# Kernel optimization log

Hardware: AMD Instinct MI355X
Metric: run time of the kernel (lower is better)

Reference implementation:

```python
import jax, jax.numpy as jnp
import numpy as np

K = 1000   # grid rows (detections from model 1, truncated to 1000)
N = 1000   # grid cols (detections from model 2)
M = 900000 # number of non-empty (overlapping) pairs
F = 7      # per-pair feature dim
SENTINEL = -9999.0


def setup_inputs() -> dict:
    key = jax.random.key(0)
    ks = jax.random.split(key, 12)
    def w(k, o, i):
        return jax.random.normal(k, (o, i), dtype=jnp.float32) * 0.05
    def b(k, o):
        return jax.random.normal(k, (o,), dtype=jnp.float32) * 0.05
    return {
        "input_1": jax.random.normal(ks[0], (1, F, 1, M), dtype=jnp.float32),
        "T_out": jnp.zeros((1, K, N), dtype=jnp.float32),
        "T_indices": jax.random.randint(ks[1], (2, M), 0, K),
        "w1": w(ks[2], 18, F),  "b1": b(ks[3], 18),
        "w2": w(ks[4], 36, 18), "b2": b(ks[5], 36),
        "w3": w(ks[6], 36, 36), "b3": b(ks[7], 36),
        "w4": w(ks[8], 1, 36),  "b4": b(ks[9], 1),
    }


def reference(input_1, T_out, T_indices, w1, b1, w2, b2, w3, b3, w4, b4):
    # 1x1 conv stack == channel matmuls on the flattened [F, M] features.
    x = input_1[0, :, 0, :]                       # [F, M]
    h = jax.nn.relu(w1 @ x + b1[:, None])         # [18, M]
    h = jax.nn.relu(w2 @ h + b2[:, None])         # [36, M]
    h = jax.nn.relu(w3 @ h + b3[:, None])         # [36, M]
    vals = (w4 @ h + b4[:, None])[0]              # [M]

    grid = jnp.full(T_out.shape, SENTINEL, dtype=T_out.dtype)  # [1, K, N]
    grid = grid.at[:, T_indices[0], T_indices[1]].set(vals[None, :])

    # MaxPool2d([1, N]) -> max over cols; MaxPool2d([K, 1]) -> max over rows.
    row_max = grid.max(axis=2).squeeze()          # [K]
    col_max = grid.max(axis=1).squeeze()          # [N]
    return (row_max, col_max)
```

## Files before the change

kernel.cpp:

```cpp
#include <hip/hip_runtime.h>
#include <stdint.h>

#define KK 1000
#define NN 1000
#define MM 900000
#define FF 7
#define SENTINEL -9999.0f

template <int N, typename F>
__device__ __forceinline__ void unroll_loop(F&& f) {
    if constexpr (N > 0) {
        unroll_loop<N - 1>(static_cast<F&&>(f));
        f(N - 1);
    }
}

__global__ __launch_bounds__(256) void init_grid(ulonglong2* __restrict__ g, int n2) {
    int i = blockIdx.x * 256 + threadIdx.x;
    if (i < n2) g[i] = make_ulonglong2(0ULL, 0ULL);
}

__global__ __launch_bounds__(256, 4) void mlp_scatter(
    const float* __restrict__ in,
    const int*   __restrict__ idx,
    const float* __restrict__ w1, const float* __restrict__ b1,
    const float* __restrict__ w2, const float* __restrict__ b2,
    const float* __restrict__ w3, const float* __restrict__ b3,
    const float* __restrict__ w4, const float* __restrict__ b4,
    unsigned long long* __restrict__ grid)
{
    int m = blockIdx.x * 256 + threadIdx.x;
    if (m >= MM) return;

    float x[FF];
    unroll_loop<FF>([&](int f) { x[f] = in[f * MM + m]; });

    float h1[18];
    unroll_loop<18>([&](int o) {
        float a = b1[o];
        unroll_loop<FF>([&](int i) { a = fmaf(w1[o * FF + i], x[i], a); });
        h1[o] = fmaxf(a, 0.0f);
    });

    float h2[36];
    unroll_loop<36>([&](int o) {
        float a = b2[o];
        unroll_loop<18>([&](int i) { a = fmaf(w2[o * 18 + i], h1[i], a); });
        h2[o] = fmaxf(a, 0.0f);
    });

    float v = b4[0];
    unroll_loop<36>([&](int o) {
        float a = b3[o];
        unroll_loop<36>([&](int i) { a = fmaf(w3[o * 36 + i], h2[i], a); });
        v = fmaf(w4[o], fmaxf(a, 0.0f), v);
    });

    int r = idx[m];
    int c = idx[MM + m];
    unsigned long long packed =
        ((unsigned long long)(unsigned)(m + 1) << 32) | (unsigned)__float_as_uint(v);
    atomicMax(&grid[r * NN + c], packed);
}

__global__ __launch_bounds__(256) void row_max_k(const unsigned long long* __restrict__ g,
                                                 float* __restrict__ out) {
    int r = blockIdx.x;
    float mx = SENTINEL;
    for (int c = threadIdx.x; c < NN; c += 256) {
        unsigned long long p = g[(size_t)r * NN + c];
        if (p) mx = fmaxf(mx, __uint_as_float((unsigned)p));
    }
    __shared__ float red[256];
    red[threadIdx.x] = mx;
    __syncthreads();
    for (int s = 128; s > 0; s >>= 1) {
        if (threadIdx.x < s) red[threadIdx.x] = fmaxf(red[threadIdx.x], red[threadIdx.x + s]);
        __syncthreads();
    }
    if (threadIdx.x == 0) out[r] = red[0];
}

#define CCHUNKS 25
#define CROWS   (KK / CCHUNKS)

__global__ __launch_bounds__(256) void col_partial(const unsigned long long* __restrict__ g,
                                                   float* __restrict__ part) {
    int n = blockIdx.x * 256 + threadIdx.x;
    if (n >= NN) return;
    int k0 = blockIdx.y * CROWS;
    float mx = SENTINEL;
    for (int k = k0; k < k0 + CROWS; ++k) {
        unsigned long long p = g[(size_t)k * NN + n];
        if (p) mx = fmaxf(mx, __uint_as_float((unsigned)p));
    }
    part[blockIdx.y * NN + n] = mx;
}

__global__ __launch_bounds__(256) void col_final(const float* __restrict__ part,
                                                 float* __restrict__ out) {
    int n = blockIdx.x * 256 + threadIdx.x;
    if (n >= NN) return;
    float mx = SENTINEL;
#pragma unroll
    for (int c = 0; c < CCHUNKS; ++c) mx = fmaxf(mx, part[c * NN + n]);
    out[KK + n] = mx;
}

extern "C" void kernel_launch(void* const* d_in, const int* in_sizes, int n_in,
                              void* d_out, int out_size, void* d_ws, size_t ws_size,
                              hipStream_t stream) {
    const float* in  = (const float*)d_in[0];
    const int*   idx = (const int*)d_in[2];
    const float* w1  = (const float*)d_in[3];
    const float* b1  = (const float*)d_in[4];
    const float* w2  = (const float*)d_in[5];
    const float* b2  = (const float*)d_in[6];
    const float* w3  = (const float*)d_in[7];
    const float* b3  = (const float*)d_in[8];
    const float* w4  = (const float*)d_in[9];
    const float* b4  = (const float*)d_in[10];

    unsigned long long* grid = (unsigned long long*)d_ws;
    float* part = (float*)((char*)d_ws + (size_t)KK * NN * 8);
    float* out  = (float*)d_out;

    const int n2 = (KK * NN) / 2;
    init_grid<<<(n2 + 255) / 256, 256, 0, stream>>>((ulonglong2*)grid, n2);

    mlp_scatter<<<(MM + 255) / 256, 256, 0, stream>>>(
        in, idx, w1, b1, w2, b2, w3, b3, w4, b4, grid);

    row_max_k<<<KK, 256, 0, stream>>>(grid, out);
    col_partial<<<dim3(4, CCHUNKS), 256, 0, stream>>>(grid, part);
    col_final<<<4, 256, 0, stream>>>(part, out);
}
```

Before: 171.9 us.

## Process four pairs per thread in MLP, vectorize weights, shuffle reduce, memset grid

Each thread of the MLP-scatter kernel now evaluates four pairs, strided by a quarter of M, so every weight load is reused across four independent FMA chains. Layer-2 and layer-3 weights are read as float2/float4, and the launch bound drops to 2 blocks per SM to leave room for the larger register footprint. The row-max reduction switches from a shared-memory tree to wave shuffles, and the grid zero-fill kernel is replaced with hipMemsetAsync. The risk is register pressure and lower occupancy, which could hide less of the memory latency.

Result: slower. 190.1 us (+10.6%).

```diff
diff --git a/kernel.cpp b/kernel.cpp
--- a/kernel.cpp
+++ b/kernel.cpp
@@ -4,23 +4,16 @@
 #define KK 1000
 #define NN 1000
 #define MM 900000
+#define QQ 225000
 #define FF 7
 #define SENTINEL -9999.0f
 
-template <int N, typename F>
-__device__ __forceinline__ void unroll_loop(F&& f) {
-    if constexpr (N > 0) {
-        unroll_loop<N - 1>(static_cast<F&&>(f));
-        f(N - 1);
-    }
-}
+#define R18(X) X(0) X(1) X(2) X(3) X(4) X(5) X(6) X(7) X(8) X(9) X(10) X(11) \
+               X(12) X(13) X(14) X(15) X(16) X(17)
+#define R36(X) R18(X) X(18) X(19) X(20) X(21) X(22) X(23) X(24) X(25) X(26) \
+               X(27) X(28) X(29) X(30) X(31) X(32) X(33) X(34) X(35)
 
-__global__ __launch_bounds__(256) void init_grid(ulonglong2* __restrict__ g, int n2) {
-    int i = blockIdx.x * 256 + threadIdx.x;
-    if (i < n2) g[i] = make_ulonglong2(0ULL, 0ULL);
-}
-
-__global__ __launch_bounds__(256, 4) void mlp_scatter(
+__global__ __launch_bounds__(256, 2) void mlp_scatter(
     const float* __restrict__ in,
     const int*   __restrict__ idx,
     const float* __restrict__ w1, const float* __restrict__ b1,
@@ -29,38 +22,78 @@
     const float* __restrict__ w4, const float* __restrict__ b4,
     unsigned long long* __restrict__ grid)
 {
-    int m = blockIdx.x * 256 + threadIdx.x;
-    if (m >= MM) return;
+    const float2* __restrict__ w2v = (const float2*)w2;
+    const float4* __restrict__ w3v = (const float4*)w3;
 
-    float x[FF];
-    unroll_loop<FF>([&](int f) { x[f] = in[f * MM + m]; });
+    int t = blockIdx.x * 256 + threadIdx.x;
+    if (t >= QQ) t = QQ - 1;
+    int m0 = t, m1 = t + QQ, m2 = t + 2 * QQ, m3 = t + 3 * QQ;
 
-    float h1[18];
-    unroll_loop<18>([&](int o) {
-        float a = b1[o];
-        unroll_loop<FF>([&](int i) { a = fmaf(w1[o * FF + i], x[i], a); });
-        h1[o] = fmaxf(a, 0.0f);
-    });
+#define XL(f) float x##f##_0 = in[(f)*MM+m0], x##f##_1 = in[(f)*MM+m1], \
+              x##f##_2 = in[(f)*MM+m2], x##f##_3 = in[(f)*MM+m3];
+    XL(0) XL(1) XL(2) XL(3) XL(4) XL(5) XL(6)
+#undef XL
 
-    float h2[36];
-    unroll_loop<36>([&](int o) {
-        float a = b2[o];
-        unroll_loop<18>([&](int i) { a = fmaf(w2[o * 18 + i], h1[i], a); });
-        h2[o] = fmaxf(a, 0.0f);
-    });
+#define T1(o,i) { float w = w1[(o)*7+(i)]; \
+    a0=fmaf(w,x##i##_0,a0); a1=fmaf(w,x##i##_1,a1); \
+    a2=fmaf(w,x##i##_2,a2); a3=fmaf(w,x##i##_3,a3); }
+#define L1(o) float h1_##o##_0,h1_##o##_1,h1_##o##_2,h1_##o##_3; { \
+    float a0=b1[o],a1=a0,a2=a0,a3=a0; \
+    T1(o,0) T1(o,1) T1(o,2) T1(o,3) T1(o,4) T1(o,5) T1(o,6) \
+    h1_##o##_0=fmaxf(a0,0.0f); h1_##o##_1=fmaxf(a1,0.0f); \
+    h1_##o##_2=fmaxf(a2,0.0f); h1_##o##_3=fmaxf(a3,0.0f); }
+    R18(L1)
+#undef L1
+#undef T1
 
-    float v = b4[0];
-    unroll_loop<36>([&](int o) {
-        float a = b3[o];
-        unroll_loop<36>([&](int i) { a = fmaf(w3[o * 36 + i], h2[i], a); });
-        v = fmaf(w4[o], fmaxf(a, 0.0f), v);
-    });
+#define T2(o,j,iA,iB) { float2 W = w2v[(o)*9+(j)]; \
+    a0=fmaf(W.x,h1_##iA##_0,a0); a1=fmaf(W.x,h1_##iA##_1,a1); \
+    a2=fmaf(W.x,h1_##iA##_2,a2); a3=fmaf(W.x,h1_##iA##_3,a3); \
+    a0=fmaf(W.y,h1_##iB##_0,a0); a1=fmaf(W.y,h1_##iB##_1,a1); \
+    a2=fmaf(W.y,h1_##iB##_2,a2); a3=fmaf(W.y,h1_##iB##_3,a3); }
+#define L2(o) float h2_##o##_0,h2_##o##_1,h2_##o##_2,h2_##o##_3; { \
+    float a0=b2[o],a1=a0,a2=a0,a3=a0; \
+    T2(o,0,0,1) T2(o,1,2,3) T2(o,2,4,5) T2(o,3,6,7) T2(o,4,8,9) \
+    T2(o,5,10,11) T2(o,6,12,13) T2(o,7,14,15) T2(o,8,16,17) \
+    h2_##o##_0=fmaxf(a0,0.0f); h2_##o##_1=fmaxf(a1,0.0f); \
+    h2_##o##_2=fmaxf(a2,0.0f); h2_##o##_3=fmaxf(a3,0.0f); }
+    R36(L2)
+#undef L2
+#undef T2
 
-    int r = idx[m];
-    int c = idx[MM + m];
-    unsigned long long packed =
-        ((unsigned long long)(unsigned)(m + 1) << 32) | (unsigned)__float_as_uint(v);
-    atomicMax(&grid[r * NN + c], packed);
+    float v0 = b4[0], v1 = v0, v2 = v0, v3 = v0;
+#define T3(o,j,iA,iB,iC,iD) { float4 W = w3v[(o)*9+(j)]; \
+    a0=fmaf(W.x,h2_##iA##_0,a0); a1=fmaf(W.x,h2_##iA##_1,a1); \
+    a2=fmaf(W.x,h2_##iA##_2,a2); a3=fmaf(W.x,h2_##iA##_3,a3); \
+    a0=fmaf(W.y,h2_##iB##_0,a0); a1=fmaf(W.y,h2_##iB##_1,a1); \
+    a2=fmaf(W.y,h2_##iB##_2,a2); a3=fmaf(W.y,h2_##iB##_3,a3); \
+    a0=fmaf(W.z,h2_##iC##_0,a0); a1=fmaf(W.z,h2_##iC##_1,a1); \
+    a2=fmaf(W.z,h2_##iC##_2,a2); a3=fmaf(W.z,h2_##iC##_3,a3); \
+    a0=fmaf(W.w,h2_##iD##_0,a0); a1=fmaf(W.w,h2_##iD##_1,a1); \
+    a2=fmaf(W.w,h2_##iD##_2,a2); a3=fmaf(W.w,h2_##iD##_3,a3); }
+#define L34(o) { float a0=b3[o],a1=a0,a2=a0,a3=a0; \
+    T3(o,0,0,1,2,3) T3(o,1,4,5,6,7) T3(o,2,8,9,10,11) T3(o,3,12,13,14,15) \
+    T3(o,4,16,17,18,19) T3(o,5,20,21,22,23) T3(o,6,24,25,26,27) \
+    T3(o,7,28,29,30,31) T3(o,8,32,33,34,35) \
+    float w = w4[o]; \
+    v0=fmaf(w,fmaxf(a0,0.0f),v0); v1=fmaf(w,fmaxf(a1,0.0f),v1); \
+    v2=fmaf(w,fmaxf(a2,0.0f),v2); v3=fmaf(w,fmaxf(a3,0.0f),v3); }
+    R36(L34)
+#undef L34
+#undef T3
+
+    int r0i = idx[m0], c0i = idx[MM + m0];
+    int r1i = idx[m1], c1i = idx[MM + m1];
+    int r2i = idx[m2], c2i = idx[MM + m2];
+    int r3i = idx[m3], c3i = idx[MM + m3];
+    atomicMax(&grid[r0i * NN + c0i],
+        ((unsigned long long)(unsigned)(m0 + 1) << 32) | (unsigned)__float_as_uint(v0));
+    atomicMax(&grid[r1i * NN + c1i],
+        ((unsigned long long)(unsigned)(m1 + 1) << 32) | (unsigned)__float_as_uint(v1));
+    atomicMax(&grid[r2i * NN + c2i],
+        ((unsigned long long)(unsigned)(m2 + 1) << 32) | (unsigned)__float_as_uint(v2));
+    atomicMax(&grid[r3i * NN + c3i],
+        ((unsigned long long)(unsigned)(m3 + 1) << 32) | (unsigned)__float_as_uint(v3));
 }
 
 __global__ __launch_bounds__(256) void row_max_k(const unsigned long long* __restrict__ g,
@@ -71,14 +104,11 @@
         unsigned long long p = g[(size_t)r * NN + c];
         if (p) mx = fmaxf(mx, __uint_as_float((unsigned)p));
     }
-    __shared__ float red[256];
-    red[threadIdx.x] = mx;
+    for (int s = 32; s > 0; s >>= 1) mx = fmaxf(mx, __shfl_down(mx, s, 64));
+    __shared__ float red[4];
+    if ((threadIdx.x & 63) == 0) red[threadIdx.x >> 6] = mx;
     __syncthreads();
-    for (int s = 128; s > 0; s >>= 1) {
-        if (threadIdx.x < s) red[threadIdx.x] = fmaxf(red[threadIdx.x], red[threadIdx.x + s]);
-        __syncthreads();
-    }
-    if (threadIdx.x == 0) out[r] = red[0];
+    if (threadIdx.x == 0) out[r] = fmaxf(fmaxf(red[0], red[1]), fmaxf(red[2], red[3]));
 }
 
 #define CCHUNKS 25
@@ -125,10 +155,9 @@
     float* part = (float*)((char*)d_ws + (size_t)KK * NN * 8);
     float* out  = (float*)d_out;
 
-    const int n2 = (KK * NN) / 2;
-    init_grid<<<(n2 + 255) / 256, 256, 0, stream>>>((ulonglong2*)grid, n2);
+    hipMemsetAsync(grid, 0, (size_t)KK * NN * 8, stream);
 
-    mlp_scatter<<<(MM + 255) / 256, 256, 0, stream>>>(
+    mlp_scatter<<<(QQ + 255) / 256, 256, 0, stream>>>(
         in, idx, w1, b1, w2, b2, w3, b3, w4, b4, grid);
 
     row_max_k<<<KK, 256, 0, stream>>>(grid, out);
```
